# Kernel tuning notes

Hardware: AMD Instinct MI355X
Metric: run time of the kernel (lower is better)

## Reference

```python
import jax, jax.numpy as jnp
import numpy as np

NUM_HEADS = 6
WS = 3

def setup_inputs() -> dict:
    key = jax.random.key(0)
    k1, k2, k3 = jax.random.split(key, 3)
    dim = 192
    x = jax.random.normal(k1, (2, dim, 48, 48, 48), dtype=jnp.float32)
    Wqkv = jax.random.normal(k2, (3 * dim, dim), dtype=jnp.float32) * (dim ** -0.5)
    Wproj = jax.random.normal(k3, (dim, dim), dtype=jnp.float32) * (dim ** -0.5)
    bproj = jnp.zeros((dim,), dtype=jnp.float32)
    return {"x": x, "Wqkv": Wqkv, "Wproj": Wproj, "bproj": bproj, "H": 384, "W": 288}

def reference(x, Wqkv, Wproj, bproj, H, W):
    b, c, h, w, d = x.shape
    xt = x.reshape(b, -1, c)                      # (B, N, C) with C = c, N = h*w*d
    B, N, C = xt.shape
    nh, ws = NUM_HEADS, WS
    hd = C // nh
    scale = hd ** -0.5
    hg, wg = H // ws, W // ws
    tg = hg * wg
    # window partition: (B, hg, ws, wg, ws, C) -> (B, hg, wg, ws, ws, C)
    xw = xt.reshape(B, hg, ws, wg, ws, C).transpose(0, 1, 3, 2, 4, 5)
    # fused QKV projection (no bias)
    qkv = jnp.einsum('bgvijc,oc->bgvijo', xw, Wqkv)          # (B,hg,wg,ws,ws,3C)
    qkv = qkv.reshape(B, tg, ws * ws, 3, nh, hd).transpose(3, 0, 1, 4, 2, 5)
    q, k, v = qkv[0], qkv[1], qkv[2]                          # (B, tg, nh, 9, hd)
    attn = jnp.einsum('bgnqd,bgnkd->bgnqk', q, k) * scale     # (B, tg, nh, 9, 9)
    attn = jax.nn.softmax(attn, axis=-1)
    out = jnp.einsum('bgnqk,bgnkd->bgnqd', attn, v)           # (B, tg, nh, 9, hd)
    out = out.transpose(0, 1, 3, 2, 4).reshape(B, hg, wg, ws, ws, C)
    out = jnp.swapaxes(out, 2, 3).reshape(B, N, C)            # un-window
    out = out @ Wproj.T + bproj
    return out.reshape(b, c, h, w, d)
```

## Files before the change

kernel.cpp:

```cpp
#include <hip/hip_runtime.h>

typedef _Float16 f16;
typedef _Float16 f16x4 __attribute__((ext_vector_type(4)));
typedef _Float16 f16x8 __attribute__((ext_vector_type(8)));
typedef float f32x4 __attribute__((ext_vector_type(4)));

#define TPB  576
#define NWIN 16
#define XS   200
#define WSS  200
#define QS   40
#define VS   264

__global__ __launch_bounds__(TPB) void lsa_mfma7(
    const float* __restrict__ x, const float* __restrict__ Wqkv,
    const float* __restrict__ Wproj, const float* __restrict__ bproj,
    float* __restrict__ out)
{
    __shared__ f16 Xh[144 * XS];
    __shared__ f16 Wh[96 * WSS];
    __shared__ f16 Qh[144 * QS];
    __shared__ f16 Kh[144 * QS];
    __shared__ f16 Vt2[32 * VS];
    __shared__ f16 AOh[144 * QS];
    __shared__ f16 Wp[192 * QS];

    const int tid  = threadIdx.x;
    const int lane = tid & 63;
    const int w    = tid >> 6;
    const int ci   = w / 3;
    const int ti   = w % 3;
    const int l15  = lane & 15;
    const int lg   = lane >> 4;

    const int  bb    = blockIdx.x / 768;
    const int  gbase = (blockIdx.x % 768) * NWIN;
    const long rb0   = (long)bb * 110592 + (long)(gbase / 96) * 864 + (long)(gbase % 96) * 3;

    const float4* Wq4 = (const float4*)Wqkv;
    const float4* Wp4 = (const float4*)Wproj;

    for (int idx = tid; idx < 144 * 48; idx += TPB) {
        int t = idx / 48, c4 = idx % 48;
        int wi = t / 9, q = t - 9 * wi;
        long grow = rb0 + wi * 3 + (q / 3) * 288 + (q % 3);
        float4 xv = ((const float4*)x)[grow * 48 + c4];
        union { f16 h[4]; ushort4 u; } tmp;
        tmp.h[0] = (f16)xv.x; tmp.h[1] = (f16)xv.y; tmp.h[2] = (f16)xv.z; tmp.h[3] = (f16)xv.w;
        *(ushort4*)&Xh[t * XS + c4 * 4] = tmp.u;
    }
    {
        int4 z = {0, 0, 0, 0};
        for (int i2 = tid; i2 < (32 * VS * 2) / 16; i2 += TPB) ((int4*)Vt2)[i2] = z;
    }
    #pragma unroll
    for (int i = 0; i < 8; ++i) {
        int l = i * TPB + tid;
        int r = l / 48, c4 = l % 48;
        float4 wv = Wq4[((r >> 5) * 192 + (r & 31)) * 48 + c4];
        union { f16 h4[4]; ushort4 u; } t;
        t.h4[0] = (f16)wv.x; t.h4[1] = (f16)wv.y; t.h4[2] = (f16)wv.z; t.h4[3] = (f16)wv.w;
        *(ushort4*)&Wh[r * WSS + c4 * 4] = t.u;
    }

    f32x4 pacc[3][4];
    #pragma unroll
    for (int a = 0; a < 3; ++a)
        #pragma unroll
        for (int bq = 0; bq < 4; ++bq)
            pacc[a][bq] = (f32x4){0.f, 0.f, 0.f, 0.f};

    __syncthreads();

    for (int h = 0; h < 6; ++h) {
        f32x4 qacc[2][3];
        #pragma unroll
        for (int c = 0; c < 2; ++c)
            #pragma unroll
            for (int t = 0; t < 3; ++t)
                qacc[c][t] = (f32x4){0.f, 0.f, 0.f, 0.f};
        #pragma unroll
        for (int kk = 0; kk < 6; ++kk) {
            f16x8 af[2], bf[3];
            #pragma unroll
            for (int c = 0; c < 2; ++c)
                af[c] = *(const f16x8*)&Wh[(16 * (ci + 3 * c) + l15) * WSS + kk * 32 + lg * 8];
            #pragma unroll
            for (int t = 0; t < 3; ++t)
                bf[t] = *(const f16x8*)&Xh[(16 * (ti + 3 * t) + l15) * XS + kk * 32 + lg * 8];
            #pragma unroll
            for (int c = 0; c < 2; ++c)
                #pragma unroll
                for (int t = 0; t < 3; ++t)
                    qacc[c][t] = __builtin_amdgcn_mfma_f32_16x16x32_f16(af[c], bf[t], qacc[c][t], 0, 0, 0);
        }
        #pragma unroll
        for (int c = 0; c < 2; ++c) {
            const int ct = ci + 3 * c;
            #pragma unroll
            for (int t = 0; t < 3; ++t) {
                const int token = 16 * (ti + 3 * t) + l15;
                f16x4 ph;
                ph[0] = (f16)qacc[c][t][0]; ph[1] = (f16)qacc[c][t][1];
                ph[2] = (f16)qacc[c][t][2]; ph[3] = (f16)qacc[c][t][3];
                if (ct < 2) {
                    *(f16x4*)&Qh[token * QS + ct * 16 + 4 * lg] = ph;
                } else if (ct < 4) {
                    *(f16x4*)&Kh[token * QS + (ct - 2) * 16 + 4 * lg] = ph;
                } else {
                    const int d0 = (ct - 4) * 16 + 4 * lg;
                    int wi = token / 9, qq = token - 9 * wi;
                    #pragma unroll
                    for (int r = 0; r < 4; ++r)
                        Vt2[(d0 + r) * VS + 16 * wi + qq] = ph[r];
                }
            }
        }
        __syncthreads();

        float4 wpv[3];
        if (tid < 512) {
            #pragma unroll
            for (int i = 0; i < 3; ++i) {
                int l = i * 512 + tid;
                int r = l / 8, c4 = l % 8;
                wpv[i] = Wp4[r * 48 + h * 8 + c4];
            }
        }
        if (h < 5) {
            #pragma unroll
            for (int i = 0; i < 8; ++i) {
                int l = i * TPB + tid;
                int r = l / 48, c4 = l % 48;
                float4 wv = Wq4[((r >> 5) * 192 + (h + 1) * 32 + (r & 31)) * 48 + c4];
                union { f16 h4[4]; ushort4 u; } t;
                t.h4[0] = (f16)wv.x; t.h4[1] = (f16)wv.y; t.h4[2] = (f16)wv.z; t.h4[3] = (f16)wv.w;
                *(ushort4*)&Wh[r * WSS + c4 * 4] = t.u;
            }
        }
        for (int wi = w; wi < NWIN; wi += 9) {
            int krow = 9 * wi + l15;
            krow = krow > 143 ? 143 : krow;
            f16x8 ak = *(const f16x8*)&Kh[krow * QS + lg * 8];
            f16x8 aq = *(const f16x8*)&Qh[krow * QS + lg * 8];
            f32x4 s = (f32x4){0.f, 0.f, 0.f, 0.f};
            s = __builtin_amdgcn_mfma_f32_16x16x32_f16(ak, aq, s, 0, 0, 0);
            float lgt[4];
            float mx = -1e30f;
            #pragma unroll
            for (int r = 0; r < 4; ++r) {
                int kx = 4 * lg + r;
                lgt[r] = (kx < 9) ? s[r] * 0.17677669529663687f : -1e30f;
                mx = fmaxf(mx, lgt[r]);
            }
            mx = fmaxf(mx, __shfl_xor(mx, 16));
            mx = fmaxf(mx, __shfl_xor(mx, 32));
            float e[4], sum = 0.f;
            #pragma unroll
            for (int r = 0; r < 4; ++r) {
                int kx = 4 * lg + r;
                e[r] = (kx < 9) ? __expf(lgt[r] - mx) : 0.f;
                sum += e[r];
            }
            sum += __shfl_xor(sum, 16);
            sum += __shfl_xor(sum, 32);
            float inv = 1.0f / sum;
            f16x4 p;
            p[0] = (f16)(e[0] * inv); p[1] = (f16)(e[1] * inv);
            p[2] = (f16)(e[2] * inv); p[3] = (f16)(e[3] * inv);
            #pragma unroll
            for (int dt = 0; dt < 2; ++dt) {
                f16x4 av = *(const f16x4*)&Vt2[(dt * 16 + l15) * VS + 16 * wi + 4 * lg];
                f32x4 o = (f32x4){0.f, 0.f, 0.f, 0.f};
                o = __builtin_amdgcn_mfma_f32_16x16x16f16(av, p, o, 0, 0, 0);
                if (l15 < 9) {
                    f16x4 oh;
                    oh[0] = (f16)o[0]; oh[1] = (f16)o[1]; oh[2] = (f16)o[2]; oh[3] = (f16)o[3];
                    *(f16x4*)&AOh[(9 * wi + l15) * QS + dt * 16 + 4 * lg] = oh;
                }
            }
        }
        if (tid < 512) {
            #pragma unroll
            for (int i = 0; i < 3; ++i) {
                int l = i * 512 + tid;
                int r = l / 8, c4 = l % 8;
                union { f16 h4[4]; ushort4 u; } t;
                t.h4[0] = (f16)wpv[i].x; t.h4[1] = (f16)wpv[i].y;
                t.h4[2] = (f16)wpv[i].z; t.h4[3] = (f16)wpv[i].w;
                *(ushort4*)&Wp[r * QS + c4 * 4] = t.u;
            }
        }
        __syncthreads();

        {
            f16x8 aof[3];
            #pragma unroll
            for (int a = 0; a < 3; ++a)
                aof[a] = *(const f16x8*)&AOh[(16 * (3 * ci + a) + l15) * QS + lg * 8];
            #pragma unroll
            for (int bq = 0; bq < 4; ++bq) {
                f16x8 bw = *(const f16x8*)&Wp[(16 * (4 * ti + bq) + l15) * QS + lg * 8];
                #pragma unroll
                for (int a = 0; a < 3; ++a)
                    pacc[a][bq] = __builtin_amdgcn_mfma_f32_16x16x32_f16(aof[a], bw, pacc[a][bq], 0, 0, 0);
            }
        }
    }

    float bv[4];
    #pragma unroll
    for (int bq = 0; bq < 4; ++bq)
        bv[bq] = bproj[16 * (4 * ti + bq) + l15];
    #pragma unroll
    for (int a = 0; a < 3; ++a) {
        #pragma unroll
        for (int r = 0; r < 4; ++r) {
            int t = 16 * (3 * ci + a) + lg * 4 + r;
            int wi = t / 9, q = t - 9 * wi;
            long grow = rb0 + wi * 3 + (q / 3) * 288 + (q % 3);
            float* dst = out + grow * 192;
            #pragma unroll
            for (int bq = 0; bq < 4; ++bq)
                dst[16 * (4 * ti + bq) + l15] = pacc[a][bq][r] + bv[bq];
        }
    }
}

extern "C" void kernel_launch(void* const* d_in, const int* in_sizes, int n_in,
                              void* d_out, int out_size, void* d_ws, size_t ws_size,
                              hipStream_t stream) {
    const float* x     = (const float*)d_in[0];
    const float* Wqkv  = (const float*)d_in[1];
    const float* Wproj = (const float*)d_in[2];
    const float* bproj = (const float*)d_in[3];
    float* out = (float*)d_out;
    lsa_mfma7<<<1536, TPB, 0, stream>>>(x, Wqkv, Wproj, bproj, out);
}
```

Measured before the change: 231.8 us.

## Pre-convert weights to padded fp16 workspace and stream them via global_load_lds

```diff
diff --git a/kernel.cpp b/kernel.cpp
--- a/kernel.cpp
+++ b/kernel.cpp
@@ -12,18 +12,46 @@
 #define QS   40
 #define VS   264
 
-__global__ __launch_bounds__(TPB) void lsa_mfma7(
-    const float* __restrict__ x, const float* __restrict__ Wqkv,
-    const float* __restrict__ Wproj, const float* __restrict__ bproj,
+#define WSQ_HALVES_PER_HEAD (96 * 200)
+#define WSP_HALVES_PER_HEAD (192 * 40)
+#define WS_NEEDED (230400 + 92160)
+
+__device__ __forceinline__ void gload16(const void* g, void* l) {
+    __builtin_amdgcn_global_load_lds(
+        (const __attribute__((address_space(1))) unsigned int*)g,
+        (__attribute__((address_space(3))) unsigned int*)l, 16, 0, 0);
+}
+
+__global__ __launch_bounds__(512) void conv_w(
+    const float* __restrict__ Wqkv, const float* __restrict__ Wproj,
+    f16* __restrict__ wsWq, f16* __restrict__ wsWp)
+{
+    int idx = blockIdx.x * 512 + threadIdx.x;
+    if (idx < 110592) {
+        int h = idx / (96 * 192), rem = idx % (96 * 192);
+        int r = rem / 192, c = rem % 192;
+        int grow = (r >> 5) * 192 + h * 32 + (r & 31);
+        wsWq[(h * 96 + r) * 200 + c] = (f16)Wqkv[grow * 192 + c];
+    } else {
+        int j = idx - 110592;
+        int h = j / (192 * 32), rem = j % (192 * 32);
+        int r = rem / 32, c = rem % 32;
+        wsWp[(h * 192 + r) * 40 + c] = (f16)Wproj[r * 192 + h * 32 + c];
+    }
+}
+
+__global__ __launch_bounds__(TPB) void lsa_mfma10(
+    const float* __restrict__ x, const f16* __restrict__ wsWq,
+    const f16* __restrict__ wsWp, const float* __restrict__ bproj,
     float* __restrict__ out)
 {
-    __shared__ f16 Xh[144 * XS];
-    __shared__ f16 Wh[96 * WSS];
-    __shared__ f16 Qh[144 * QS];
-    __shared__ f16 Kh[144 * QS];
-    __shared__ f16 Vt2[32 * VS];
-    __shared__ f16 AOh[144 * QS];
-    __shared__ f16 Wp[192 * QS];
+    __shared__ __attribute__((aligned(16))) f16 Xh[144 * XS];
+    __shared__ __attribute__((aligned(16))) f16 Wh[96 * WSS];
+    __shared__ __attribute__((aligned(16))) f16 Qh[144 * QS];
+    __shared__ __attribute__((aligned(16))) f16 Kh[144 * QS];
+    __shared__ __attribute__((aligned(16))) f16 Vt2[32 * VS];
+    __shared__ __attribute__((aligned(16))) f16 AOh[144 * QS];
+    __shared__ __attribute__((aligned(16))) f16 Wp[192 * QS];
 
     const int tid  = threadIdx.x;
     const int lane = tid & 63;
@@ -37,9 +65,8 @@
     const int  gbase = (blockIdx.x % 768) * NWIN;
     const long rb0   = (long)bb * 110592 + (long)(gbase / 96) * 864 + (long)(gbase % 96) * 3;
 
-    const float4* Wq4 = (const float4*)Wqkv;
-    const float4* Wp4 = (const float4*)Wproj;
-
+    for (int l = tid; l < 2400; l += TPB)
+        gload16(wsWq + l * 8, (char*)Wh + l * 16);
     for (int idx = tid; idx < 144 * 48; idx += TPB) {
         int t = idx / 48, c4 = idx % 48;
         int wi = t / 9, q = t - 9 * wi;
@@ -52,15 +79,6 @@
     {
         int4 z = {0, 0, 0, 0};
         for (int i2 = tid; i2 < (32 * VS * 2) / 16; i2 += TPB) ((int4*)Vt2)[i2] = z;
-    }
-    #pragma unroll
-    for (int i = 0; i < 8; ++i) {
-        int l = i * TPB + tid;
-        int r = l / 48, c4 = l % 48;
-        float4 wv = Wq4[((r >> 5) * 192 + (r & 31)) * 48 + c4];
-        union { f16 h4[4]; ushort4 u; } t;
-        t.h4[0] = (f16)wv.x; t.h4[1] = (f16)wv.y; t.h4[2] = (f16)wv.z; t.h4[3] = (f16)wv.w;
-        *(ushort4*)&Wh[r * WSS + c4 * 4] = t.u;
     }
 
     f32x4 pacc[3][4];
@@ -118,26 +136,13 @@
         }
         __syncthreads();
 
-        float4 wpv[3];
-        if (tid < 512) {
-            #pragma unroll
-            for (int i = 0; i < 3; ++i) {
-                int l = i * 512 + tid;
-                int r = l / 8, c4 = l % 8;
-                wpv[i] = Wp4[r * 48 + h * 8 + c4];
-            }
-        }
         if (h < 5) {
-            #pragma unroll
-            for (int i = 0; i < 8; ++i) {
-                int l = i * TPB + tid;
-                int r = l / 48, c4 = l % 48;
-                float4 wv = Wq4[((r >> 5) * 192 + (h + 1) * 32 + (r & 31)) * 48 + c4];
-                union { f16 h4[4]; ushort4 u; } t;
-                t.h4[0] = (f16)wv.x; t.h4[1] = (f16)wv.y; t.h4[2] = (f16)wv.z; t.h4[3] = (f16)wv.w;
-                *(ushort4*)&Wh[r * WSS + c4 * 4] = t.u;
-            }
-        }
+            for (int l = tid; l < 2400; l += TPB)
+                gload16(wsWq + (h + 1) * WSQ_HALVES_PER_HEAD + l * 8, (char*)Wh + l * 16);
+        }
+        for (int l = tid; l < 960; l += TPB)
+            gload16(wsWp + h * WSP_HALVES_PER_HEAD + l * 8, (char*)Wp + l * 16);
+
         for (int wi = w; wi < NWIN; wi += 9) {
             int krow = 9 * wi + l15;
             krow = krow > 143 ? 143 : krow;
@@ -180,6 +185,210 @@
                 }
             }
         }
+        __syncthreads();
+
+        {
+            f16x8 aof[3];
+            #pragma unroll
+            for (int a = 0; a < 3; ++a)
+                aof[a] = *(const f16x8*)&AOh[(16 * (3 * ci + a) + l15) * QS + lg * 8];
+            #pragma unroll
+            for (int bq = 0; bq < 4; ++bq) {
+                f16x8 bw = *(const f16x8*)&Wp[(16 * (4 * ti + bq) + l15) * QS + lg * 8];
+                #pragma unroll
+                for (int a = 0; a < 3; ++a)
+                    pacc[a][bq] = __builtin_amdgcn_mfma_f32_16x16x32_f16(aof[a], bw, pacc[a][bq], 0, 0, 0);
+            }
+        }
+    }
+
+    float bv[4];
+    #pragma unroll
+    for (int bq = 0; bq < 4; ++bq)
+        bv[bq] = bproj[16 * (4 * ti + bq) + l15];
+    #pragma unroll
+    for (int a = 0; a < 3; ++a) {
+        #pragma unroll
+        for (int r = 0; r < 4; ++r) {
+            int t = 16 * (3 * ci + a) + lg * 4 + r;
+            int wi = t / 9, q = t - 9 * wi;
+            long grow = rb0 + wi * 3 + (q / 3) * 288 + (q % 3);
+            float* dst = out + grow * 192;
+            #pragma unroll
+            for (int bq = 0; bq < 4; ++bq)
+                dst[16 * (4 * ti + bq) + l15] = pacc[a][bq][r] + bv[bq];
+        }
+    }
+}
+
+__global__ __launch_bounds__(TPB) void lsa_mfma7(
+    const float* __restrict__ x, const float* __restrict__ Wqkv,
+    const float* __restrict__ Wproj, const float* __restrict__ bproj,
+    float* __restrict__ out)
+{
+    __shared__ f16 Xh[144 * XS];
+    __shared__ f16 Wh[96 * WSS];
+    __shared__ f16 Qh[144 * QS];
+    __shared__ f16 Kh[144 * QS];
+    __shared__ f16 Vt2[32 * VS];
+    __shared__ f16 AOh[144 * QS];
+    __shared__ f16 Wp[192 * QS];
+
+    const int tid  = threadIdx.x;
+    const int lane = tid & 63;
+    const int w    = tid >> 6;
+    const int ci   = w / 3;
+    const int ti   = w % 3;
+    const int l15  = lane & 15;
+    const int lg   = lane >> 4;
+
+    const int  bb    = blockIdx.x / 768;
+    const int  gbase = (blockIdx.x % 768) * NWIN;
+    const long rb0   = (long)bb * 110592 + (long)(gbase / 96) * 864 + (long)(gbase % 96) * 3;
+
+    const float4* Wq4 = (const float4*)Wqkv;
+    const float4* Wp4 = (const float4*)Wproj;
+
+    for (int idx = tid; idx < 144 * 48; idx += TPB) {
+        int t = idx / 48, c4 = idx % 48;
+        int wi = t / 9, q = t - 9 * wi;
+        long grow = rb0 + wi * 3 + (q / 3) * 288 + (q % 3);
+        float4 xv = ((const float4*)x)[grow * 48 + c4];
+        union { f16 h[4]; ushort4 u; } tmp;
+        tmp.h[0] = (f16)xv.x; tmp.h[1] = (f16)xv.y; tmp.h[2] = (f16)xv.z; tmp.h[3] = (f16)xv.w;
+        *(ushort4*)&Xh[t * XS + c4 * 4] = tmp.u;
+    }
+    {
+        int4 z = {0, 0, 0, 0};
+        for (int i2 = tid; i2 < (32 * VS * 2) / 16; i2 += TPB) ((int4*)Vt2)[i2] = z;
+    }
+    #pragma unroll
+    for (int i = 0; i < 8; ++i) {
+        int l = i * TPB + tid;
+        int r = l / 48, c4 = l % 48;
+        float4 wv = Wq4[((r >> 5) * 192 + (r & 31)) * 48 + c4];
+        union { f16 h4[4]; ushort4 u; } t;
+        t.h4[0] = (f16)wv.x; t.h4[1] = (f16)wv.y; t.h4[2] = (f16)wv.z; t.h4[3] = (f16)wv.w;
+        *(ushort4*)&Wh[r * WSS + c4 * 4] = t.u;
+    }
+
+    f32x4 pacc[3][4];
+    #pragma unroll
+    for (int a = 0; a < 3; ++a)
+        #pragma unroll
+        for (int bq = 0; bq < 4; ++bq)
+            pacc[a][bq] = (f32x4){0.f, 0.f, 0.f, 0.f};
+
+    __syncthreads();
+
+    for (int h = 0; h < 6; ++h) {
+        f32x4 qacc[2][3];
+        #pragma unroll
+        for (int c = 0; c < 2; ++c)
+            #pragma unroll
+            for (int t = 0; t < 3; ++t)
+                qacc[c][t] = (f32x4){0.f, 0.f, 0.f, 0.f};
+        #pragma unroll
+        for (int kk = 0; kk < 6; ++kk) {
+            f16x8 af[2], bf[3];
+            #pragma unroll
+            for (int c = 0; c < 2; ++c)
+                af[c] = *(const f16x8*)&Wh[(16 * (ci + 3 * c) + l15) * WSS + kk * 32 + lg * 8];
+            #pragma unroll
+            for (int t = 0; t < 3; ++t)
+                bf[t] = *(const f16x8*)&Xh[(16 * (ti + 3 * t) + l15) * XS + kk * 32 + lg * 8];
+            #pragma unroll
+            for (int c = 0; c < 2; ++c)
+                #pragma unroll
+                for (int t = 0; t < 3; ++t)
+                    qacc[c][t] = __builtin_amdgcn_mfma_f32_16x16x32_f16(af[c], bf[t], qacc[c][t], 0, 0, 0);
+        }
+        #pragma unroll
+        for (int c = 0; c < 2; ++c) {
+            const int ct = ci + 3 * c;
+            #pragma unroll
+            for (int t = 0; t < 3; ++t) {
+                const int token = 16 * (ti + 3 * t) + l15;
+                f16x4 ph;
+                ph[0] = (f16)qacc[c][t][0]; ph[1] = (f16)qacc[c][t][1];
+                ph[2] = (f16)qacc[c][t][2]; ph[3] = (f16)qacc[c][t][3];
+                if (ct < 2) {
+                    *(f16x4*)&Qh[token * QS + ct * 16 + 4 * lg] = ph;
+                } else if (ct < 4) {
+                    *(f16x4*)&Kh[token * QS + (ct - 2) * 16 + 4 * lg] = ph;
+                } else {
+                    const int d0 = (ct - 4) * 16 + 4 * lg;
+                    int wi = token / 9, qq = token - 9 * wi;
+                    #pragma unroll
+                    for (int r = 0; r < 4; ++r)
+                        Vt2[(d0 + r) * VS + 16 * wi + qq] = ph[r];
+                }
+            }
+        }
+        __syncthreads();
+
+        float4 wpv[3];
+        if (tid < 512) {
+            #pragma unroll
+            for (int i = 0; i < 3; ++i) {
+                int l = i * 512 + tid;
+                int r = l / 8, c4 = l % 8;
+                wpv[i] = Wp4[r * 48 + h * 8 + c4];
+            }
+        }
+        if (h < 5) {
+            #pragma unroll
+            for (int i = 0; i < 8; ++i) {
+                int l = i * TPB + tid;
+                int r = l / 48, c4 = l % 48;
+                float4 wv = Wq4[((r >> 5) * 192 + (h + 1) * 32 + (r & 31)) * 48 + c4];
+                union { f16 h4[4]; ushort4 u; } t;
+                t.h4[0] = (f16)wv.x; t.h4[1] = (f16)wv.y; t.h4[2] = (f16)wv.z; t.h4[3] = (f16)wv.w;
+                *(ushort4*)&Wh[r * WSS + c4 * 4] = t.u;
+            }
+        }
+        for (int wi = w; wi < NWIN; wi += 9) {
+            int krow = 9 * wi + l15;
+            krow = krow > 143 ? 143 : krow;
+            f16x8 ak = *(const f16x8*)&Kh[krow * QS + lg * 8];
+            f16x8 aq = *(const f16x8*)&Qh[krow * QS + lg * 8];
+            f32x4 s = (f32x4){0.f, 0.f, 0.f, 0.f};
+            s = __builtin_amdgcn_mfma_f32_16x16x32_f16(ak, aq, s, 0, 0, 0);
+            float lgt[4];
+            float mx = -1e30f;
+            #pragma unroll
+            for (int r = 0; r < 4; ++r) {
+                int kx = 4 * lg + r;
+                lgt[r] = (kx < 9) ? s[r] * 0.17677669529663687f : -1e30f;
+                mx = fmaxf(mx, lgt[r]);
+            }
+            mx = fmaxf(mx, __shfl_xor(mx, 16));
+            mx = fmaxf(mx, __shfl_xor(mx, 32));
+            float e[4], sum = 0.f;
+            #pragma unroll
+            for (int r = 0; r < 4; ++r) {
+                int kx = 4 * lg + r;
+                e[r] = (kx < 9) ? __expf(lgt[r] - mx) : 0.f;
+                sum += e[r];
+            }
+            sum += __shfl_xor(sum, 16);
+            sum += __shfl_xor(sum, 32);
+            float inv = 1.0f / sum;
+            f16x4 p;
+            p[0] = (f16)(e[0] * inv); p[1] = (f16)(e[1] * inv);
+            p[2] = (f16)(e[2] * inv); p[3] = (f16)(e[3] * inv);
+            #pragma unroll
+            for (int dt = 0; dt < 2; ++dt) {
+                f16x4 av = *(const f16x4*)&Vt2[(dt * 16 + l15) * VS + 16 * wi + 4 * lg];
+                f32x4 o = (f32x4){0.f, 0.f, 0.f, 0.f};
+                o = __builtin_amdgcn_mfma_f32_16x16x16f16(av, p, o, 0, 0, 0);
+                if (l15 < 9) {
+                    f16x4 oh;
+                    oh[0] = (f16)o[0]; oh[1] = (f16)o[1]; oh[2] = (f16)o[2]; oh[3] = (f16)o[3];
+                    *(f16x4*)&AOh[(9 * wi + l15) * QS + dt * 16 + 4 * lg] = oh;
+                }
+            }
+        }
         if (tid < 512) {
             #pragma unroll
             for (int i = 0; i < 3; ++i) {
@@ -235,5 +444,12 @@
     const float* Wproj = (const float*)d_in[2];
     const float* bproj = (const float*)d_in[3];
     float* out = (float*)d_out;
-    lsa_mfma7<<<1536, TPB, 0, stream>>>(x, Wqkv, Wproj, bproj, out);
+    if (ws_size >= (size_t)WS_NEEDED && d_ws != nullptr) {
+        f16* wsWq = (f16*)d_ws;
+        f16* wsWp = (f16*)((char*)d_ws + 230400);
+        conv_w<<<288, 512, 0, stream>>>(Wqkv, Wproj, wsWq, wsWp);
+        lsa_mfma10<<<1536, TPB, 0, stream>>>(x, wsWq, wsWp, bproj, out);
+    } else {
+        lsa_mfma7<<<1536, TPB, 0, stream>>>(x, Wqkv, Wproj, bproj, out);
+    }
 }
```

Result: faster. 205.2 us (-11.5%).
